# Kernel tuning notes

Hardware: AMD Instinct MI355X
Metric: run time of the kernel (lower is better)

The kernel has to match this reference:

```python
import jax, jax.numpy as jnp
import numpy as np
from jax import lax

EPS = 1e-08

def _sobel_edges(x, sx, sy):
    # x: [B, C, H, W]; depthwise 3x3 conv per channel, SAME padding.
    B, C, H, W = x.shape
    kx = jnp.tile(sx, (C, 1, 1, 1))  # [C,1,3,3] OIHW with feature_group_count=C
    ky = jnp.tile(sy, (C, 1, 1, 1))
    dn = ('NCHW', 'OIHW', 'NCHW')
    gx = lax.conv_general_dilated(x, kx, (1, 1), 'SAME',
                                  dimension_numbers=dn, feature_group_count=C)
    gy = lax.conv_general_dilated(x, ky, (1, 1), 'SAME',
                                  dimension_numbers=dn, feature_group_count=C)
    return jnp.sqrt(gx * gx + gy * gy + EPS)

def setup_inputs() -> dict:
    key = jax.random.key(0)
    k1, k2 = jax.random.split(key)
    B, C, H, W = 16, 8, 512, 512
    source_latent = jax.random.normal(k1, (B, C, H, W), dtype=jnp.float32)
    edited_latent = jax.random.normal(k2, (B, C, H, W), dtype=jnp.float32)
    sx = jnp.array([[-1., 0., 1.], [-2., 0., 2.], [-1., 0., 1.]], dtype=jnp.float32).reshape(1, 1, 3, 3)
    sy = jnp.array([[-1., -2., -1.], [0., 0., 0.], [1., 2., 1.]], dtype=jnp.float32).reshape(1, 1, 3, 3)
    return {"source_latent": source_latent, "edited_latent": edited_latent, "sx": sx, "sy": sy}

def reference(source_latent, edited_latent, sx, sy):
    e_src = _sobel_edges(source_latent, sx, sy)
    e_edit = _sobel_edges(edited_latent, sx, sy)
    diff = e_edit - e_src
    return jnp.mean(diff * diff)
```

## Files before the change

kernel.cpp:

```cpp
#include <hip/hip_runtime.h>


#define EPS 1e-8f

constexpr int W_DIM  = 512;
constexpr int H_DIM  = 512;
constexpr int NIMG   = 128;
constexpr int ROWS   = 32;
constexpr int CHUNKS = H_DIM / ROWS;
constexpr int TPB    = 128;
constexpr int NBLK   = NIMG * CHUNKS;
constexpr double TOTAL_ELEMS = 33554432.0;

struct RowBuf { float4 s, e; float ss, es; };

__global__ __launch_bounds__(TPB) void edge_loss_stage1(
    const float* __restrict__ src, const float* __restrict__ edt,
    float* __restrict__ partial)
{
    const int blk  = blockIdx.x;
    const int img  = blk / CHUNKS;
    const int r0   = (blk % CHUNKS) * ROWS;
    const int wv   = threadIdx.x >> 6;
    const int lane = threadIdx.x & 63;
    const int c0   = threadIdx.x * 4;

    const float* simg = src + (size_t)img * (H_DIM * W_DIM);
    const float* eimg = edt + (size_t)img * (H_DIM * W_DIM);

    const bool seam_active = (wv == 0) ? (lane == 63) : (lane == 0);
    const int  seamcol     = (wv == 0) ? 256 : 255;

    float sP0[4], sP1[4], sQ0[4], sQ1[4];
    float eP0[4], eP1[4], eQ0[4], eQ1[4];
    float acc = 0.f;

    auto issue = [&](int h, RowBuf& rb) {
        int hc = h < 0 ? 0 : (h >= H_DIM ? H_DIM - 1 : h);
        const float* srow = simg + (size_t)hc * W_DIM;
        const float* erow = eimg + (size_t)hc * W_DIM;
        rb.s = *reinterpret_cast<const float4*>(srow + c0);
        rb.e = *reinterpret_cast<const float4*>(erow + c0);
        rb.ss = 0.f; rb.es = 0.f;
        if (seam_active) { rb.ss = srow[seamcol]; rb.es = erow[seamcol]; }
    };

    auto halos = [&](const RowBuf& rb, float sp[6], float ep[6]) {
        float slT = __shfl_up(rb.s.w, 1);
        float srT = __shfl_down(rb.s.x, 1);
        float elT = __shfl_up(rb.e.w, 1);
        float erT = __shfl_down(rb.e.x, 1);
        sp[0] = (lane == 0)  ? rb.ss : slT;
        sp[5] = (lane == 63) ? rb.ss : srT;
        ep[0] = (lane == 0)  ? rb.es : elT;
        ep[5] = (lane == 63) ? rb.es : erT;
        sp[1]=rb.s.x; sp[2]=rb.s.y; sp[3]=rb.s.z; sp[4]=rb.s.w;
        ep[1]=rb.e.x; ep[2]=rb.e.y; ep[3]=rb.e.z; ep[4]=rb.e.w;
    };

    auto consume = [&](const RowBuf& rb, int h) {
        if (h < H_DIM) {
            float sp[6], ep[6];
            halos(rb, sp, ep);
            #pragma unroll
            for (int i = 0; i < 4; ++i) {
                float a  = sp[i+2] - sp[i];
                float b  = sp[i] + 2.f*sp[i+1] + sp[i+2];
                float gx = sP0[i] + a;
                float gy = b - sQ0[i];
                sP0[i] = fmaf(2.f, a, sP1[i]); sP1[i] = a;
                sQ0[i] = sQ1[i]; sQ1[i] = b;
                float es = __builtin_amdgcn_sqrtf(fmaf(gx, gx, fmaf(gy, gy, EPS)));
                float a2  = ep[i+2] - ep[i];
                float b2  = ep[i] + 2.f*ep[i+1] + ep[i+2];
                float gx2 = eP0[i] + a2;
                float gy2 = b2 - eQ0[i];
                eP0[i] = fmaf(2.f, a2, eP1[i]); eP1[i] = a2;
                eQ0[i] = eQ1[i]; eQ1[i] = b2;
                float ee = __builtin_amdgcn_sqrtf(fmaf(gx2, gx2, fmaf(gy2, gy2, EPS)));
                float d = ee - es;
                acc = fmaf(d, d, acc);
            }
        } else {
            #pragma unroll
            for (int i = 0; i < 4; ++i) {
                float gx = sP0[i], gy = -sQ0[i];
                sP0[i] = sP1[i]; sP1[i] = 0.f; sQ0[i] = sQ1[i]; sQ1[i] = 0.f;
                float es = __builtin_amdgcn_sqrtf(fmaf(gx, gx, fmaf(gy, gy, EPS)));
                float gx2 = eP0[i], gy2 = -eQ0[i];
                eP0[i] = eP1[i]; eP1[i] = 0.f; eQ0[i] = eQ1[i]; eQ1[i] = 0.f;
                float ee = __builtin_amdgcn_sqrtf(fmaf(gx2, gx2, fmaf(gy2, gy2, EPS)));
                float d = ee - es;
                acc = fmaf(d, d, acc);
            }
        }
    };

    RowBuf bA0, bA1, bB0, bB1;
    issue(r0 - 1, bA0);
    issue(r0,     bA1);
    issue(r0 + 1, bB0);
    issue(r0 + 2, bB1);

    if (r0 > 0) {
        float sp[6], ep[6];
        halos(bA0, sp, ep);
        #pragma unroll
        for (int i = 0; i < 4; ++i) {
            sP0[i] = sp[i+2] - sp[i];
            sQ0[i] = sp[i] + 2.f*sp[i+1] + sp[i+2];
            eP0[i] = ep[i+2] - ep[i];
            eQ0[i] = ep[i] + 2.f*ep[i+1] + ep[i+2];
        }
    } else {
        #pragma unroll
        for (int i = 0; i < 4; ++i) { sP0[i]=0.f; sQ0[i]=0.f; eP0[i]=0.f; eQ0[i]=0.f; }
    }
    {
        float sp[6], ep[6];
        halos(bA1, sp, ep);
        #pragma unroll
        for (int i = 0; i < 4; ++i) {
            float a  = sp[i+2] - sp[i];
            sP0[i] = fmaf(2.f, a, sP0[i]); sP1[i] = a;
            sQ1[i] = sp[i] + 2.f*sp[i+1] + sp[i+2];
            float a2 = ep[i+2] - ep[i];
            eP0[i] = fmaf(2.f, a2, eP0[i]); eP1[i] = a2;
            eQ1[i] = ep[i] + 2.f*ep[i+1] + ep[i+2];
        }
    }

    int h = r0 + 1;
    #pragma unroll 1
    for (int k = 0; k < ROWS / 4; ++k, h += 4) {
        if (h + 2 <= r0 + ROWS) issue(h + 2, bA0);
        if (h + 3 <= r0 + ROWS) issue(h + 3, bA1);
        consume(bB0, h);
        consume(bB1, h + 1);
        if (h + 4 <= r0 + ROWS) issue(h + 4, bB0);
        if (h + 5 <= r0 + ROWS) issue(h + 5, bB1);
        consume(bA0, h + 2);
        consume(bA1, h + 3);
    }

    #pragma unroll
    for (int off = 32; off > 0; off >>= 1)
        acc += __shfl_down(acc, off);
    __shared__ float wsum[TPB / 64];
    if (lane == 0) wsum[wv] = acc;
    __syncthreads();
    if (threadIdx.x == 0) {
        float tot = 0.f;
        #pragma unroll
        for (int i = 0; i < TPB / 64; ++i) tot += wsum[i];
        partial[blk] = tot;
    }
}

__global__ __launch_bounds__(256) void edge_loss_stage2(
    const float* __restrict__ partial, float* __restrict__ out, int nparts)
{
    double acc = 0.0;
    for (int i = threadIdx.x; i < nparts; i += 256)
        acc += (double)partial[i];
    #pragma unroll
    for (int off = 32; off > 0; off >>= 1)
        acc += __shfl_down(acc, off);
    __shared__ double wsum[4];
    const int wid  = threadIdx.x >> 6;
    const int lane = threadIdx.x & 63;
    if (lane == 0) wsum[wid] = acc;
    __syncthreads();
    if (threadIdx.x == 0) {
        double t = 0.0;
        #pragma unroll
        for (int i = 0; i < 4; ++i) t += wsum[i];
        out[0] = (float)(t / TOTAL_ELEMS);
    }
}

extern "C" void kernel_launch(void* const* d_in, const int* in_sizes, int n_in,
                              void* d_out, int out_size, void* d_ws, size_t ws_size,
                              hipStream_t stream) {
    const float* src = (const float*)d_in[0];
    const float* edt = (const float*)d_in[1];
    float* out     = (float*)d_out;
    float* partial = (float*)d_ws;

    edge_loss_stage1<<<dim3(NBLK), dim3(TPB), 0, stream>>>(src, edt, partial);
    edge_loss_stage2<<<dim3(1), dim3(256), 0, stream>>>(partial, out, NBLK);
}
```

Measured before the change: 50.88 us.

## Pack Sobel math into float2 vectors and expand squared edge difference algebraically

Rewrites the per-pixel Sobel computation with two-wide float vectors so the compiler can emit packed FP32 instructions (v_pk_add/mul/fma), halving VALU instruction count for the stencil. It also replaces (sqrt(S)-sqrt(E))^2 with S+E-2*sqrt(S*E), cutting two square roots per pixel to one. The algebraic form loses precision through cancellation when S and E are close, and still needs per-lane sqrt. The kernel is meant to be compute-bound enough that fewer ALU ops matter.

Result: slower. 57.01 us (+12.0%).

```diff
diff --git a/kernel.cpp b/kernel.cpp
--- a/kernel.cpp
+++ b/kernel.cpp
@@ -1,5 +1,7 @@
 #include <hip/hip_runtime.h>
 
+
+typedef float v2f __attribute__((ext_vector_type(2)));
 
 #define EPS 1e-8f
 
@@ -31,9 +33,9 @@
     const bool seam_active = (wv == 0) ? (lane == 63) : (lane == 0);
     const int  seamcol     = (wv == 0) ? 256 : 255;
 
-    float sP0[4], sP1[4], sQ0[4], sQ1[4];
-    float eP0[4], eP1[4], eQ0[4], eQ1[4];
-    float acc = 0.f;
+    v2f sP0[2], sP1[2], sQ0[2], sQ1[2];
+    v2f eP0[2], eP1[2], eQ0[2], eQ1[2];
+    v2f accv; accv.x = 0.f; accv.y = 0.f;
 
     auto issue = [&](int h, RowBuf& rb) {
         int hc = h < 0 ? 0 : (h >= H_DIM ? H_DIM - 1 : h);
@@ -45,54 +47,77 @@
         if (seam_active) { rb.ss = srow[seamcol]; rb.es = erow[seamcol]; }
     };
 
-    auto halos = [&](const RowBuf& rb, float sp[6], float ep[6]) {
+    auto rowAB = [&](const RowBuf& rb,
+                     v2f& sa0, v2f& sa1, v2f& sb0, v2f& sb1,
+                     v2f& ea0, v2f& ea1, v2f& eb0, v2f& eb1) {
         float slT = __shfl_up(rb.s.w, 1);
         float srT = __shfl_down(rb.s.x, 1);
         float elT = __shfl_up(rb.e.w, 1);
         float erT = __shfl_down(rb.e.x, 1);
-        sp[0] = (lane == 0)  ? rb.ss : slT;
-        sp[5] = (lane == 63) ? rb.ss : srT;
-        ep[0] = (lane == 0)  ? rb.es : elT;
-        ep[5] = (lane == 63) ? rb.es : erT;
-        sp[1]=rb.s.x; sp[2]=rb.s.y; sp[3]=rb.s.z; sp[4]=rb.s.w;
-        ep[1]=rb.e.x; ep[2]=rb.e.y; ep[3]=rb.e.z; ep[4]=rb.e.w;
+        float sl = (lane == 0)  ? rb.ss : slT;
+        float sr = (lane == 63) ? rb.ss : srT;
+        float el = (lane == 0)  ? rb.es : elT;
+        float er = (lane == 63) ? rb.es : erT;
+
+        v2f L01, L23, L45, M12, M34;
+        L01.x = sl;      L01.y = rb.s.x;
+        L23.x = rb.s.y;  L23.y = rb.s.z;
+        L45.x = rb.s.w;  L45.y = sr;
+        M12.x = rb.s.x;  M12.y = rb.s.y;
+        M34.x = rb.s.z;  M34.y = rb.s.w;
+        sa0 = L23 - L01;               sa1 = L45 - L23;
+        sb0 = (L01 + L23) + 2.0f*M12;  sb1 = (L23 + L45) + 2.0f*M34;
+
+        v2f K01, K23, K45, N12, N34;
+        K01.x = el;      K01.y = rb.e.x;
+        K23.x = rb.e.y;  K23.y = rb.e.z;
+        K45.x = rb.e.w;  K45.y = er;
+        N12.x = rb.e.x;  N12.y = rb.e.y;
+        N34.x = rb.e.z;  N34.y = rb.e.w;
+        ea0 = K23 - K01;               ea1 = K45 - K23;
+        eb0 = (K01 + K23) + 2.0f*N12;  eb1 = (K23 + K45) + 2.0f*N34;
+    };
+
+    auto accum = [&](v2f S, v2f E) {
+        v2f m = S * E;
+        v2f r;
+        r.x = __builtin_amdgcn_sqrtf(m.x);
+        r.y = __builtin_amdgcn_sqrtf(m.y);
+        accv += (S + E) - 2.0f*r;
     };
 
     auto consume = [&](const RowBuf& rb, int h) {
         if (h < H_DIM) {
-            float sp[6], ep[6];
-            halos(rb, sp, ep);
-            #pragma unroll
-            for (int i = 0; i < 4; ++i) {
-                float a  = sp[i+2] - sp[i];
-                float b  = sp[i] + 2.f*sp[i+1] + sp[i+2];
-                float gx = sP0[i] + a;
-                float gy = b - sQ0[i];
-                sP0[i] = fmaf(2.f, a, sP1[i]); sP1[i] = a;
-                sQ0[i] = sQ1[i]; sQ1[i] = b;
-                float es = __builtin_amdgcn_sqrtf(fmaf(gx, gx, fmaf(gy, gy, EPS)));
-                float a2  = ep[i+2] - ep[i];
-                float b2  = ep[i] + 2.f*ep[i+1] + ep[i+2];
-                float gx2 = eP0[i] + a2;
-                float gy2 = b2 - eQ0[i];
-                eP0[i] = fmaf(2.f, a2, eP1[i]); eP1[i] = a2;
-                eQ0[i] = eQ1[i]; eQ1[i] = b2;
-                float ee = __builtin_amdgcn_sqrtf(fmaf(gx2, gx2, fmaf(gy2, gy2, EPS)));
-                float d = ee - es;
-                acc = fmaf(d, d, acc);
-            }
+            v2f sa0, sa1, sb0, sb1, ea0, ea1, eb0, eb1;
+            rowAB(rb, sa0, sa1, sb0, sb1, ea0, ea1, eb0, eb1);
+
+            v2f sgx0 = sP0[0] + sa0,  sgx1 = sP0[1] + sa1;
+            v2f sgy0 = sb0 - sQ0[0],  sgy1 = sb1 - sQ0[1];
+            sP0[0] = 2.0f*sa0 + sP1[0]; sP1[0] = sa0;
+            sP0[1] = 2.0f*sa1 + sP1[1]; sP1[1] = sa1;
+            sQ0[0] = sQ1[0]; sQ1[0] = sb0;
+            sQ0[1] = sQ1[1]; sQ1[1] = sb1;
+
+            v2f egx0 = eP0[0] + ea0,  egx1 = eP0[1] + ea1;
+            v2f egy0 = eb0 - eQ0[0],  egy1 = eb1 - eQ0[1];
+            eP0[0] = 2.0f*ea0 + eP1[0]; eP1[0] = ea0;
+            eP0[1] = 2.0f*ea1 + eP1[1]; eP1[1] = ea1;
+            eQ0[0] = eQ1[0]; eQ1[0] = eb0;
+            eQ0[1] = eQ1[1]; eQ1[1] = eb1;
+
+            v2f S0 = sgx0*sgx0 + sgy0*sgy0 + EPS;
+            v2f S1 = sgx1*sgx1 + sgy1*sgy1 + EPS;
+            v2f E0 = egx0*egx0 + egy0*egy0 + EPS;
+            v2f E1 = egx1*egx1 + egy1*egy1 + EPS;
+            accum(S0, E0);
+            accum(S1, E1);
         } else {
-            #pragma unroll
-            for (int i = 0; i < 4; ++i) {
-                float gx = sP0[i], gy = -sQ0[i];
-                sP0[i] = sP1[i]; sP1[i] = 0.f; sQ0[i] = sQ1[i]; sQ1[i] = 0.f;
-                float es = __builtin_amdgcn_sqrtf(fmaf(gx, gx, fmaf(gy, gy, EPS)));
-                float gx2 = eP0[i], gy2 = -eQ0[i];
-                eP0[i] = eP1[i]; eP1[i] = 0.f; eQ0[i] = eQ1[i]; eQ1[i] = 0.f;
-                float ee = __builtin_amdgcn_sqrtf(fmaf(gx2, gx2, fmaf(gy2, gy2, EPS)));
-                float d = ee - es;
-                acc = fmaf(d, d, acc);
-            }
+            v2f S0 = sP0[0]*sP0[0] + sQ0[0]*sQ0[0] + EPS;
+            v2f S1 = sP0[1]*sP0[1] + sQ0[1]*sQ0[1] + EPS;
+            v2f E0 = eP0[0]*eP0[0] + eQ0[0]*eQ0[0] + EPS;
+            v2f E1 = eP0[1]*eP0[1] + eQ0[1]*eQ0[1] + EPS;
+            accum(S0, E0);
+            accum(S1, E1);
         }
     };
 
@@ -103,31 +128,22 @@
     issue(r0 + 2, bB1);
 
     if (r0 > 0) {
-        float sp[6], ep[6];
-        halos(bA0, sp, ep);
-        #pragma unroll
-        for (int i = 0; i < 4; ++i) {
-            sP0[i] = sp[i+2] - sp[i];
-            sQ0[i] = sp[i] + 2.f*sp[i+1] + sp[i+2];
-            eP0[i] = ep[i+2] - ep[i];
-            eQ0[i] = ep[i] + 2.f*ep[i+1] + ep[i+2];
-        }
+        v2f sa0, sa1, sb0, sb1, ea0, ea1, eb0, eb1;
+        rowAB(bA0, sa0, sa1, sb0, sb1, ea0, ea1, eb0, eb1);
+        sP0[0] = sa0; sP0[1] = sa1; sQ0[0] = sb0; sQ0[1] = sb1;
+        eP0[0] = ea0; eP0[1] = ea1; eQ0[0] = eb0; eQ0[1] = eb1;
     } else {
-        #pragma unroll
-        for (int i = 0; i < 4; ++i) { sP0[i]=0.f; sQ0[i]=0.f; eP0[i]=0.f; eQ0[i]=0.f; }
+        v2f z; z.x = 0.f; z.y = 0.f;
+        sP0[0]=z; sP0[1]=z; sQ0[0]=z; sQ0[1]=z;
+        eP0[0]=z; eP0[1]=z; eQ0[0]=z; eQ0[1]=z;
     }
     {
-        float sp[6], ep[6];
-        halos(bA1, sp, ep);
-        #pragma unroll
-        for (int i = 0; i < 4; ++i) {
-            float a  = sp[i+2] - sp[i];
-            sP0[i] = fmaf(2.f, a, sP0[i]); sP1[i] = a;
-            sQ1[i] = sp[i] + 2.f*sp[i+1] + sp[i+2];
-            float a2 = ep[i+2] - ep[i];
-            eP0[i] = fmaf(2.f, a2, eP0[i]); eP1[i] = a2;
-            eQ1[i] = ep[i] + 2.f*ep[i+1] + ep[i+2];
-        }
+        v2f sa0, sa1, sb0, sb1, ea0, ea1, eb0, eb1;
+        rowAB(bA1, sa0, sa1, sb0, sb1, ea0, ea1, eb0, eb1);
+        sP0[0] += 2.0f*sa0; sP1[0] = sa0; sQ1[0] = sb0;
+        sP0[1] += 2.0f*sa1; sP1[1] = sa1; sQ1[1] = sb1;
+        eP0[0] += 2.0f*ea0; eP1[0] = ea0; eQ1[0] = eb0;
+        eP0[1] += 2.0f*ea1; eP1[1] = ea1; eQ1[1] = eb1;
     }
 
     int h = r0 + 1;
@@ -143,6 +159,7 @@
         consume(bA1, h + 3);
     }
 
+    float acc = accv.x + accv.y;
     #pragma unroll
     for (int off = 32; off > 0; off >>= 1)
         acc += __shfl_down(acc, off);
```
